# Optimization experiments

Measured on AMD Instinct MI355X. Metric: run time of the kernel, lower is better.

Reference implementation:

```python
import jax, jax.numpy as jnp
import numpy as np

N, H, V = 4096, 1024, 16384


def setup_inputs() -> dict:
    key = jax.random.key(0)
    k1, k2, k3, k4 = jax.random.split(key, 4)
    _input = jax.random.normal(k1, (N, H), dtype=jnp.float32)
    weight = jax.random.normal(k2, (V, H), dtype=jnp.float32) * (1.0 / np.sqrt(H))
    target = jax.random.normal(k3, (N, V), dtype=jnp.float32)
    bias = jax.random.normal(k4, (V,), dtype=jnp.float32)
    return {"_input": _input, "weight": weight, "target": target, "bias": bias}


def reference(_input, weight, target, bias):
    # Fused linear + MSE with reduction='mean':
    # logits = _input @ weight.T + bias  -> (N, V)
    # loss = mean((logits - target)**2) over all N*V elements
    logits = jnp.einsum("nh,vh->nv", _input, weight) + bias
    diff = logits - target
    return jnp.mean(diff * diff)
```

## Files before the change

### kernel.cpp

```cpp
#include <hip/hip_runtime.h>
#include <hip/hip_bf16.h>
#include <stdint.h>

#define N_ 4096
#define H_ 1024
#define V_ 16384

using i32x8  = __attribute__((ext_vector_type(8))) int;
using f32x16 = __attribute__((ext_vector_type(16))) float;

__global__ void cast2_f32_to_fp8(const float* __restrict__ in0, uint8_t* __restrict__ out0,
                                 const float* __restrict__ in1, uint8_t* __restrict__ out1,
                                 int nblk0) {
    const float* in;
    uint8_t* out;
    int bid;
    if (blockIdx.x < (unsigned)nblk0) { in = in0; out = out0; bid = blockIdx.x; }
    else                              { in = in1; out = out1; bid = blockIdx.x - nblk0; }
    size_t i = ((size_t)bid * blockDim.x + threadIdx.x) * 8;
    float4 a = *(const float4*)(in + i);
    float4 b = *(const float4*)(in + i + 4);
    int lo = __builtin_amdgcn_cvt_pk_fp8_f32(a.x, a.y, 0, 0);
    lo     = __builtin_amdgcn_cvt_pk_fp8_f32(a.z, a.w, lo, 1);
    int hi = __builtin_amdgcn_cvt_pk_fp8_f32(b.x, b.y, 0, 0);
    hi     = __builtin_amdgcn_cvt_pk_fp8_f32(b.z, b.w, hi, 1);
    *(int2*)(out + i) = make_int2(lo, hi);
}

#define BM 128
#define BN 128
#define BK 128

__global__ __launch_bounds__(256, 2) void gemm_mse(
    const uint8_t* __restrict__ A8,
    const uint8_t* __restrict__ W8,
    const float*  __restrict__ target,
    const float*  __restrict__ bias,
    float* __restrict__ partials)
{
    extern __shared__ __align__(16) uint8_t smem[];
    uint8_t* As = smem;
    uint8_t* Bs = smem + 32768;
    __shared__ float red[4];

    const int tid  = threadIdx.x;
    const int w    = tid >> 6;
    const int lane = tid & 63;
    const int l32  = lane & 31;
    const int half = lane >> 5;
    const int wm   = w >> 1;
    const int wn   = w & 1;

    const int flat = blockIdx.x;
    const int xcd  = flat & 7;
    const int idx  = flat >> 3;
    const int tx   = xcd * 16 + (idx & 15);
    const int ty   = idx >> 4;

    const int rowBase = ty * BM;
    const int colBase = tx * BN;

    f32x16 acc[2][2];
#pragma unroll
    for (int i = 0; i < 2; ++i)
#pragma unroll
        for (int j = 0; j < 2; ++j)
#pragma unroll
            for (int r = 0; r < 16; ++r) acc[i][j][r] = 0.f;

    const int ldrow = lane >> 2;
    const int ldkq  = (lane & 3) ^ ((ldrow + (ldrow >> 2)) & 3);

    const int rl  = lane & 15;
    const int rcb = (lane >> 4) & 1;
    const int fl  = (rl + (rl >> 2)) & 3;
    int aOff[2][2], bOff[2][2];
#pragma unroll
    for (int i = 0; i < 2; ++i)
#pragma unroll
        for (int c = 0; c < 2; ++c) {
            const int slot = rl * 4 + (((half << 1) + c) ^ fl);
            aOff[i][c] = ((wm * 2 + i) * 2 + rcb) * 1024 + slot * 16;
            bOff[i][c] = ((wn * 2 + i) * 2 + rcb) * 1024 + slot * 16;
        }

    float biasj[2];
#pragma unroll
    for (int j = 0; j < 2; ++j) biasj[j] = bias[colBase + wn * 64 + j * 32 + l32];

    auto STAGE = [&](int t, int buf) {
        const int kT = t * BK;
#pragma unroll
        for (int h = 0; h < 2; ++h) {
#pragma unroll
            for (int c = 0; c < 2; ++c) {
                const int cid  = w * 2 + c;
                const int kOff = kT + h * 64 + ldkq * 16;
                const uint8_t* ga = A8 + (size_t)(rowBase + cid * 16 + ldrow) * H_ + kOff;
                __builtin_amdgcn_global_load_lds(
                    (const __attribute__((address_space(1))) void*)ga,
                    (__attribute__((address_space(3))) void*)(As + buf * 16384 + h * 8192 + cid * 1024),
                    16, 0, 0);
                const uint8_t* gb = W8 + (size_t)(colBase + cid * 16 + ldrow) * H_ + kOff;
                __builtin_amdgcn_global_load_lds(
                    (const __attribute__((address_space(1))) void*)gb,
                    (__attribute__((address_space(3))) void*)(Bs + buf * 16384 + h * 8192 + cid * 1024),
                    16, 0, 0);
            }
        }
    };

    float tgt0[16][2], tgt1[16][2];

    STAGE(0, 0);
    asm volatile("s_waitcnt vmcnt(0)" ::: "memory");
    __builtin_amdgcn_s_barrier();
    asm volatile("" ::: "memory");

    int cur = 0;
    for (int t = 0; t < 8; ++t) {
        if (t < 7) STAGE(t + 1, cur ^ 1);
        asm volatile("" ::: "memory");
        if (t == 6) {
#pragma unroll
            for (int r = 0; r < 16; ++r) {
                const int row = (r & 3) + 8 * (r >> 2) + 4 * half;
                const float* trow = target + (size_t)(rowBase + wm * 64 + 0 * 32 + row) * V_
                                    + colBase + wn * 64 + l32;
                tgt0[r][0] = trow[0];
                tgt0[r][1] = trow[32];
            }
        }
        if (t == 7) {
#pragma unroll
            for (int r = 0; r < 16; ++r) {
                const int row = (r & 3) + 8 * (r >> 2) + 4 * half;
                const float* trow = target + (size_t)(rowBase + wm * 64 + 1 * 32 + row) * V_
                                    + colBase + wn * 64 + l32;
                tgt1[r][0] = trow[0];
                tgt1[r][1] = trow[32];
            }
        }

        const uint8_t* aB = As + cur * 16384;
        const uint8_t* bB = Bs + cur * 16384;
#pragma unroll
        for (int h = 0; h < 2; ++h) {
            i32x8 af[2], bq[2];
#pragma unroll
            for (int i = 0; i < 2; ++i) {
                int4 a0 = *(const int4*)(aB + h * 8192 + aOff[i][0]);
                int4 a1 = *(const int4*)(aB + h * 8192 + aOff[i][1]);
                af[i][0] = a0.x; af[i][1] = a0.y; af[i][2] = a0.z; af[i][3] = a0.w;
                af[i][4] = a1.x; af[i][5] = a1.y; af[i][6] = a1.z; af[i][7] = a1.w;
                int4 b0 = *(const int4*)(bB + h * 8192 + bOff[i][0]);
                int4 b1 = *(const int4*)(bB + h * 8192 + bOff[i][1]);
                bq[i][0] = b0.x; bq[i][1] = b0.y; bq[i][2] = b0.z; bq[i][3] = b0.w;
                bq[i][4] = b1.x; bq[i][5] = b1.y; bq[i][6] = b1.z; bq[i][7] = b1.w;
            }
            __builtin_amdgcn_s_setprio(1);
#pragma unroll
            for (int i = 0; i < 2; ++i)
#pragma unroll
                for (int j = 0; j < 2; ++j)
                    acc[i][j] = __builtin_amdgcn_mfma_scale_f32_32x32x64_f8f6f4(
                        af[i], bq[j], acc[i][j],
                        0 , 0 ,
                        0, 0x7F7F7F7F,
                        0, 0x7F7F7F7F);
            __builtin_amdgcn_s_setprio(0);
        }

        if (t < 7) {
            asm volatile("s_waitcnt vmcnt(0)" ::: "memory");
            __builtin_amdgcn_s_barrier();
            asm volatile("" ::: "memory");
        }
        cur ^= 1;
    }

    float sum = 0.f;
#pragma unroll
    for (int r = 0; r < 16; ++r) {
#pragma unroll
        for (int j = 0; j < 2; ++j) {
            float d = acc[0][j][r] + biasj[j] - tgt0[r][j];
            sum += d * d;
        }
    }
#pragma unroll
    for (int r = 0; r < 16; ++r) {
#pragma unroll
        for (int j = 0; j < 2; ++j) {
            float d = acc[1][j][r] + biasj[j] - tgt1[r][j];
            sum += d * d;
        }
    }

#pragma unroll
    for (int off = 32; off; off >>= 1) sum += __shfl_down(sum, off, 64);
    if (lane == 0) red[w] = sum;
    __syncthreads();
    if (tid == 0)
        partials[flat] = red[0] + red[1] + red[2] + red[3];
}

__global__ void finalize_kernel(const float* __restrict__ partials, float* __restrict__ out, int n) {
    float s = 0.f;
    for (int i = threadIdx.x; i < n; i += 256) s += partials[i];
#pragma unroll
    for (int off = 32; off; off >>= 1) s += __shfl_down(s, off, 64);
    __shared__ float red[4];
    const int w = threadIdx.x >> 6, lane = threadIdx.x & 63;
    if (lane == 0) red[w] = s;
    __syncthreads();
    if (threadIdx.x == 0)
        out[0] = (red[0] + red[1] + red[2] + red[3]) * (1.0f / ((float)N_ * (float)V_));
}

extern "C" void kernel_launch(void* const* d_in, const int* in_sizes, int n_in,
                              void* d_out, int out_size, void* d_ws, size_t ws_size,
                              hipStream_t stream) {
    const float* input  = (const float*)d_in[0];
    const float* weight = (const float*)d_in[1];
    const float* target = (const float*)d_in[2];
    const float* bias   = (const float*)d_in[3];
    float* out = (float*)d_out;

    uint8_t* A8 = (uint8_t*)d_ws;
    uint8_t* W8 = A8 + (size_t)N_ * H_;
    float* partials = (float*)(W8 + (size_t)V_ * H_);

    const int nblk0 = (N_ * H_) / (256 * 8);
    const int nblk1 = (V_ * H_) / (256 * 8);
    cast2_f32_to_fp8<<<nblk0 + nblk1, 256, 0, stream>>>(input, A8, weight, W8, nblk0);

    const int nblocks = (V_ / BN) * (N_ / BM);
    gemm_mse<<<nblocks, 256, 65536, stream>>>(A8, W8, target, bias, partials);

    finalize_kernel<<<1, 256, 0, stream>>>(partials, out, nblocks);
}
```

Before: 455.4 us.

## Load weight fragments directly from global into registers, bypassing LDS

The weight (B) operand is no longer staged through shared memory. Each lane loads its MFMA fragment straight from global memory into registers at the start of every k-step, and only the A operand stays in double-buffered LDS. This halves LDS footprint and LDS traffic, which could allow more resident blocks. The cost is that the B loads are issued at the top of each iteration with no prefetch, so global latency may be exposed, and B is no longer shared across the two wm warps, which doubles global/L2 reads of W.

```diff
diff --git a/kernel.cpp b/kernel.cpp
--- a/kernel.cpp
+++ b/kernel.cpp
@@ -38,9 +38,7 @@
     const float*  __restrict__ bias,
     float* __restrict__ partials)
 {
-    extern __shared__ __align__(16) uint8_t smem[];
-    uint8_t* As = smem;
-    uint8_t* Bs = smem + 32768;
+    __shared__ __align__(16) uint8_t As[2][16384];
     __shared__ float red[4];
 
     const int tid  = threadIdx.x;
@@ -74,15 +72,19 @@
     const int rl  = lane & 15;
     const int rcb = (lane >> 4) & 1;
     const int fl  = (rl + (rl >> 2)) & 3;
-    int aOff[2][2], bOff[2][2];
+    int aOff[2][2];
 #pragma unroll
     for (int i = 0; i < 2; ++i)
 #pragma unroll
         for (int c = 0; c < 2; ++c) {
             const int slot = rl * 4 + (((half << 1) + c) ^ fl);
             aOff[i][c] = ((wm * 2 + i) * 2 + rcb) * 1024 + slot * 16;
-            bOff[i][c] = ((wn * 2 + i) * 2 + rcb) * 1024 + slot * 16;
-        }
+        }
+
+    const uint8_t* pB[2];
+#pragma unroll
+    for (int j = 0; j < 2; ++j)
+        pB[j] = W8 + (size_t)(colBase + wn * 64 + j * 32 + l32) * H_ + (half * 32);
 
     float biasj[2];
 #pragma unroll
@@ -99,12 +101,7 @@
                 const uint8_t* ga = A8 + (size_t)(rowBase + cid * 16 + ldrow) * H_ + kOff;
                 __builtin_amdgcn_global_load_lds(
                     (const __attribute__((address_space(1))) void*)ga,
-                    (__attribute__((address_space(3))) void*)(As + buf * 16384 + h * 8192 + cid * 1024),
-                    16, 0, 0);
-                const uint8_t* gb = W8 + (size_t)(colBase + cid * 16 + ldrow) * H_ + kOff;
-                __builtin_amdgcn_global_load_lds(
-                    (const __attribute__((address_space(1))) void*)gb,
-                    (__attribute__((address_space(3))) void*)(Bs + buf * 16384 + h * 8192 + cid * 1024),
+                    (__attribute__((address_space(3))) void*)(&As[buf][0] + h * 8192 + cid * 1024),
                     16, 0, 0);
             }
         }
@@ -119,6 +116,15 @@
 
     int cur = 0;
     for (int t = 0; t < 8; ++t) {
+        int4 bg[2][2][2];
+#pragma unroll
+        for (int h = 0; h < 2; ++h)
+#pragma unroll
+            for (int j = 0; j < 2; ++j)
+#pragma unroll
+                for (int c = 0; c < 2; ++c)
+                    bg[h][j][c] = *(const int4*)(pB[j] + t * BK + h * 64 + c * 16);
+
         if (t < 7) STAGE(t + 1, cur ^ 1);
         asm volatile("" ::: "memory");
         if (t == 6) {
@@ -142,8 +148,7 @@
             }
         }
 
-        const uint8_t* aB = As + cur * 16384;
-        const uint8_t* bB = Bs + cur * 16384;
+        const uint8_t* aB = &As[cur][0];
 #pragma unroll
         for (int h = 0; h < 2; ++h) {
             i32x8 af[2], bq[2];
@@ -153,10 +158,13 @@
                 int4 a1 = *(const int4*)(aB + h * 8192 + aOff[i][1]);
                 af[i][0] = a0.x; af[i][1] = a0.y; af[i][2] = a0.z; af[i][3] = a0.w;
                 af[i][4] = a1.x; af[i][5] = a1.y; af[i][6] = a1.z; af[i][7] = a1.w;
-                int4 b0 = *(const int4*)(bB + h * 8192 + bOff[i][0]);
-                int4 b1 = *(const int4*)(bB + h * 8192 + bOff[i][1]);
-                bq[i][0] = b0.x; bq[i][1] = b0.y; bq[i][2] = b0.z; bq[i][3] = b0.w;
-                bq[i][4] = b1.x; bq[i][5] = b1.y; bq[i][6] = b1.z; bq[i][7] = b1.w;
+            }
+#pragma unroll
+            for (int j = 0; j < 2; ++j) {
+                bq[j][0] = bg[h][j][0].x; bq[j][1] = bg[h][j][0].y;
+                bq[j][2] = bg[h][j][0].z; bq[j][3] = bg[h][j][0].w;
+                bq[j][4] = bg[h][j][1].x; bq[j][5] = bg[h][j][1].y;
+                bq[j][6] = bg[h][j][1].z; bq[j][7] = bg[h][j][1].w;
             }
             __builtin_amdgcn_s_setprio(1);
 #pragma unroll
@@ -236,7 +244,7 @@
     cast2_f32_to_fp8<<<nblk0 + nblk1, 256, 0, stream>>>(input, A8, weight, W8, nblk0);
 
     const int nblocks = (V_ / BN) * (N_ / BM);
-    gemm_mse<<<nblocks, 256, 65536, stream>>>(A8, W8, target, bias, partials);
+    gemm_mse<<<nblocks, 256, 0, stream>>>(A8, W8, target, bias, partials);
 
     finalize_kernel<<<1, 256, 0, stream>>>(partials, out, nblocks);
 }
```

Measured after the change: 510.2 us. 12.0% more time.
